# Kernel tuning notes

Hardware: AMD Instinct MI355X
Metric: run time of the kernel (lower is better)

The kernel has to match this reference:

```python
import jax, jax.numpy as jnp
import numpy as np

B, N, IN_DIM, HID = 16, 2048, 128, 128
EPS = 1e-5


def _layer(x, W, b, g, beta):
    # x: (B, N, d_in) -> (B, N, HID)
    h = jnp.einsum('bnd,dh->bnh', x, W) + b
    mu = jnp.mean(h, axis=-1, keepdims=True)
    var = jnp.mean((h - mu) ** 2, axis=-1, keepdims=True)
    h = (h - mu) * jax.lax.rsqrt(var + EPS) * g + beta
    return jax.nn.relu(h)


def setup_inputs() -> dict:
    key = jax.random.key(0)
    ks = jax.random.split(key, 8)
    x = jax.random.normal(ks[0], (B, N, IN_DIM), dtype=jnp.float32)
    adj = jax.random.uniform(ks[1], (B, N, N), dtype=jnp.float32)
    inp = {'x': x, 'adj': adj}
    dims = [IN_DIM, HID, HID]
    for i in range(3):
        d_in = dims[i]
        scale = 1.0 / np.sqrt(d_in)
        inp[f'W{i}'] = jax.random.uniform(ks[2 + i], (d_in, HID), dtype=jnp.float32, minval=-scale, maxval=scale)
        inp[f'b{i}'] = jax.random.uniform(ks[5 + i], (HID,), dtype=jnp.float32, minval=-scale, maxval=scale)
        inp[f'g{i}'] = jnp.ones((HID,), dtype=jnp.float32)
        inp[f'be{i}'] = jnp.zeros((HID,), dtype=jnp.float32)
    return inp


def reference(x, adj, W0, b0, g0, be0, W1, b1, g1, be1, W2, b2, g2, be2):
    params = [(W0, b0, g0, be0), (W1, b1, g1, be1), (W2, b2, g2, be2)]
    h = x
    for (W, b, g, beta) in params:
        h_agg = jnp.einsum('bnm,bmd->bnd', adj, h)  # dense adjacency aggregation
        h = _layer(h_agg, W, b, g, beta)
    return h
```

## Files before the change

kernel.cpp:

```cpp
#include <hip/hip_runtime.h>
#include <hip/hip_bf16.h>

typedef __bf16 bf16;
typedef __bf16 bf16x4 __attribute__((ext_vector_type(4)));
typedef __bf16 bf16x8 __attribute__((ext_vector_type(8)));
typedef float  f32x4  __attribute__((ext_vector_type(4)));

static constexpr int NB   = 16;
static constexpr int NN   = 2048;
static constexpr int HID  = 128;

__global__ __launch_bounds__(256) void prep_wt(const float* __restrict__ W0,
                                               const float* __restrict__ W1,
                                               const float* __restrict__ W2,
                                               bf16* __restrict__ WT) {
    int l = blockIdx.x;
    const float* W = (l == 0) ? W0 : (l == 1) ? W1 : W2;
    bf16* out = WT + l * 128 * 128;
    int tid = threadIdx.x;
#pragma unroll
    for (int i = 0; i < 64; ++i) {
        int idx = i * 256 + tid;
        int k = idx >> 7, n = idx & 127;
        out[n * 128 + k] = (bf16)W[idx];
    }
}

template<typename TA>
__global__ __launch_bounds__(256) void small_gemm(const TA* __restrict__ A,
                                                  const bf16* __restrict__ WT,
                                                  bf16* __restrict__ tmpT) {
    __shared__ bf16 smem[2 * 128 * 72];
    bf16* As = smem;
    bf16* Bs = smem + 128 * 72;

    const int tid  = threadIdx.x;
    const int wave = tid >> 6, lane = tid & 63;
    const int c0 = lane & 15, q = lane >> 4;
    const int blk = blockIdx.x;
    const int row_g0 = blk * 128;

    f32x4 acc[2][8] = {};

    for (int kk = 0; kk < 2; ++kk) {
        const int k0 = kk * 64;
        if constexpr (sizeof(TA) == 4) {
#pragma unroll
            for (int i = 0; i < 8; ++i) {
                int flat = i * 1024 + tid * 4;
                int row = flat >> 6, col = flat & 63;
                f32x4 v = *(const f32x4*)(A + (size_t)(row_g0 + row) * 128 + k0 + col);
                bf16x4 o = { (bf16)v.x, (bf16)v.y, (bf16)v.z, (bf16)v.w };
                *(bf16x4*)(As + row * 72 + col) = o;
            }
        } else {
#pragma unroll
            for (int i = 0; i < 4; ++i) {
                int flat = i * 2048 + tid * 8;
                int row = flat >> 6, col = flat & 63;
                bf16x8 v = *(const bf16x8*)((const bf16*)A + (size_t)(row_g0 + row) * 128 + k0 + col);
                *(bf16x8*)(As + row * 72 + col) = v;
            }
        }
#pragma unroll
        for (int i = 0; i < 4; ++i) {
            int flat = i * 2048 + tid * 8;
            int row = flat >> 6, col = flat & 63;
            bf16x8 v = *(const bf16x8*)(WT + (size_t)row * 128 + k0 + col);
            *(bf16x8*)(Bs + row * 72 + col) = v;
        }
        __syncthreads();
#pragma unroll
        for (int ks = 0; ks < 2; ++ks) {
            bf16x8 af[2];
#pragma unroll
            for (int mt = 0; mt < 2; ++mt)
                af[mt] = *(const bf16x8*)(As + (wave * 32 + mt * 16 + c0) * 72 + ks * 32 + q * 8);
#pragma unroll
            for (int nt = 0; nt < 8; ++nt) {
                bf16x8 bfr = *(const bf16x8*)(Bs + (nt * 16 + c0) * 72 + ks * 32 + q * 8);
#pragma unroll
                for (int mt = 0; mt < 2; ++mt)
                    acc[mt][nt] = __builtin_amdgcn_mfma_f32_16x16x32_bf16(af[mt], bfr, acc[mt][nt], 0, 0, 0);
            }
        }
        __syncthreads();
    }

    bf16* Cs = smem;
#pragma unroll
    for (int mt = 0; mt < 2; ++mt) {
        int mbase = wave * 32 + mt * 16 + q * 4;
#pragma unroll
        for (int nt = 0; nt < 8; ++nt) {
            int n = nt * 16 + c0;
#pragma unroll
            for (int r = 0; r < 4; ++r)
                Cs[n * 136 + mbase + r] = (bf16)acc[mt][nt][r];
        }
    }
    __syncthreads();
    const int b    = blk >> 4;
    const int row0 = (blk & 15) * 128;
    bf16* outp = tmpT + (size_t)b * 128 * 2048;
#pragma unroll
    for (int i = 0; i < 8; ++i) {
        int flat = i * 2048 + tid * 8;
        int n = flat >> 7, m = flat & 127;
        bf16x8 v = *(const bf16x8*)(Cs + n * 136 + m);
        *(bf16x8*)(outp + (size_t)n * 2048 + row0 + m) = v;
    }
}

template<int AMODE, bool OUTF32>
__global__ __launch_bounds__(256) void big_gemm(const float* __restrict__ Af,
                                                bf16* __restrict__ adjB,
                                                const bf16* __restrict__ Bt,
                                                const float* __restrict__ bias,
                                                const float* __restrict__ gamma,
                                                const float* __restrict__ betap,
                                                bf16* __restrict__ outB,
                                                float* __restrict__ outF) {
    __shared__ bf16 As[128 * 72];
    __shared__ bf16 Bs[128 * 72];

    const int tid  = threadIdx.x;
    const int wave = tid >> 6, lane = tid & 63;
    const int c0 = lane & 15, q = lane >> 4;
    const int b  = blockIdx.z;
    const int m0 = blockIdx.x * 128;
    const size_t abase = (size_t)b * 2048 * 2048;
    const bf16* Btb = Bt + (size_t)b * 128 * 2048;

    f32x4 acc[2][8] = {};

    for (int kk = 0; kk < 32; ++kk) {
        const int k0 = kk * 64;
        if constexpr (AMODE <= 1) {
#pragma unroll
            for (int i = 0; i < 8; ++i) {
                int flat = i * 1024 + tid * 4;
                int row = flat >> 6, col = flat & 63;
                f32x4 v = *(const f32x4*)(Af + abase + (size_t)(m0 + row) * 2048 + k0 + col);
                bf16x4 o = { (bf16)v.x, (bf16)v.y, (bf16)v.z, (bf16)v.w };
                *(bf16x4*)(As + row * 72 + col) = o;
                if constexpr (AMODE == 1)
                    *(bf16x4*)(adjB + abase + (size_t)(m0 + row) * 2048 + k0 + col) = o;
            }
        } else {
#pragma unroll
            for (int i = 0; i < 4; ++i) {
                int flat = i * 2048 + tid * 8;
                int row = flat >> 6, col = flat & 63;
                bf16x8 v = *(const bf16x8*)(adjB + abase + (size_t)(m0 + row) * 2048 + k0 + col);
                *(bf16x8*)(As + row * 72 + col) = v;
            }
        }
#pragma unroll
        for (int i = 0; i < 4; ++i) {
            int flat = i * 2048 + tid * 8;
            int row = flat >> 6, col = flat & 63;
            bf16x8 v = *(const bf16x8*)(Btb + (size_t)row * 2048 + k0 + col);
            *(bf16x8*)(Bs + row * 72 + col) = v;
        }
        __syncthreads();
#pragma unroll
        for (int ks = 0; ks < 2; ++ks) {
            bf16x8 af[2];
#pragma unroll
            for (int mt = 0; mt < 2; ++mt)
                af[mt] = *(const bf16x8*)(As + (wave * 32 + mt * 16 + c0) * 72 + ks * 32 + q * 8);
#pragma unroll
            for (int nt = 0; nt < 8; ++nt) {
                bf16x8 bfr = *(const bf16x8*)(Bs + (nt * 16 + c0) * 72 + ks * 32 + q * 8);
#pragma unroll
                for (int mt = 0; mt < 2; ++mt)
                    acc[mt][nt] = __builtin_amdgcn_mfma_f32_16x16x32_bf16(af[mt], bfr, acc[mt][nt], 0, 0, 0);
            }
        }
        __syncthreads();
    }

    float bv[8], gv[8], bev[8];
#pragma unroll
    for (int nt = 0; nt < 8; ++nt) {
        int n = nt * 16 + c0;
        bv[nt] = bias[n]; gv[nt] = gamma[n]; bev[nt] = betap[n];
    }
#pragma unroll
    for (int mt = 0; mt < 2; ++mt) {
#pragma unroll
        for (int r = 0; r < 4; ++r) {
            float s1 = 0.f, s2 = 0.f;
            float v[8];
#pragma unroll
            for (int nt = 0; nt < 8; ++nt) {
                float x = acc[mt][nt][r] + bv[nt];
                v[nt] = x; s1 += x; s2 += x * x;
            }
#pragma unroll
            for (int off = 1; off < 16; off <<= 1) {
                s1 += __shfl_xor(s1, off);
                s2 += __shfl_xor(s2, off);
            }
            float mu  = s1 * (1.f / 128.f);
            float var = s2 * (1.f / 128.f) - mu * mu;
            float rs  = rsqrtf(var + 1e-5f);
            int m = m0 + wave * 32 + mt * 16 + q * 4 + r;
            size_t rowoff = ((size_t)b * 2048 + m) * 128;
#pragma unroll
            for (int nt = 0; nt < 8; ++nt) {
                int n = nt * 16 + c0;
                float o = (v[nt] - mu) * rs * gv[nt] + bev[nt];
                o = fmaxf(o, 0.f);
                if constexpr (OUTF32) outF[rowoff + n] = o;
                else                  outB[rowoff + n] = (bf16)o;
            }
        }
    }
}

extern "C" void kernel_launch(void* const* d_in, const int* in_sizes, int n_in,
                              void* d_out, int out_size, void* d_ws, size_t ws_size,
                              hipStream_t stream) {
    const float* x   = (const float*)d_in[0];
    const float* adj = (const float*)d_in[1];
    const float* W[3]  = {(const float*)d_in[2],  (const float*)d_in[6],  (const float*)d_in[10]};
    const float* bb[3] = {(const float*)d_in[3],  (const float*)d_in[7],  (const float*)d_in[11]};
    const float* gg[3] = {(const float*)d_in[4],  (const float*)d_in[8],  (const float*)d_in[12]};
    const float* be[3] = {(const float*)d_in[5],  (const float*)d_in[9],  (const float*)d_in[13]};

    char* ws = (char*)d_ws;
    size_t off = 0;
    bf16* WT   = (bf16*)(ws + off); off += (size_t)3 * 128 * 128 * 2;
    off = (off + 255) & ~(size_t)255;
    bf16* tmpT = (bf16*)(ws + off); off += (size_t)NB * 128 * NN * 2;
    bf16* hB   = (bf16*)(ws + off); off += (size_t)NB * NN * 128 * 2;
    bf16* adjB = (bf16*)(ws + off); off += (size_t)NB * NN * NN * 2;
    const bool use_adjB = (ws_size >= off);

    float* outF = (float*)d_out;

    prep_wt<<<3, 256, 0, stream>>>(W[0], W[1], W[2], WT);

    dim3 bg(16, 1, 16);
    small_gemm<float><<<256, 256, 0, stream>>>(x, WT, tmpT);
    if (use_adjB)
        big_gemm<1, false><<<bg, 256, 0, stream>>>(adj, adjB, tmpT, bb[0], gg[0], be[0], hB, nullptr);
    else
        big_gemm<0, false><<<bg, 256, 0, stream>>>(adj, adjB, tmpT, bb[0], gg[0], be[0], hB, nullptr);
    small_gemm<bf16><<<256, 256, 0, stream>>>(hB, WT + 128 * 128, tmpT);
    if (use_adjB)
        big_gemm<2, false><<<bg, 256, 0, stream>>>(adj, adjB, tmpT, bb[1], gg[1], be[1], hB, nullptr);
    else
        big_gemm<0, false><<<bg, 256, 0, stream>>>(adj, adjB, tmpT, bb[1], gg[1], be[1], hB, nullptr);
    small_gemm<bf16><<<256, 256, 0, stream>>>(hB, WT + 2 * 128 * 128, tmpT);
    if (use_adjB)
        big_gemm<2, true><<<bg, 256, 0, stream>>>(adj, adjB, tmpT, bb[2], gg[2], be[2], nullptr, outF);
    else
        big_gemm<0, true><<<bg, 256, 0, stream>>>(adj, adjB, tmpT, bb[2], gg[2], be[2], nullptr, outF);
}
```

Measured before the change: 585.4 us.

## Split-K big GEMM with direct-to-LDS loads, swizzled LDS, separate reduce+LayerNorm

The adjacency is now converted to bf16 once in a dedicated pass. The big aggregation GEMM splits K in two across blockIdx.y, which doubles the grid from 256 to 512 blocks on a 256-CU part. It loads tiles with global_load_lds into an XOR-swizzled LDS layout and uses a 2x2 wave tiling with 4x4 MFMA fragments per wave. Partial sums go to an fp32 workspace, and a new reduce kernel adds the two halves and applies bias, LayerNorm and ReLU. This adds fp32 partial-sum traffic, extra launches and a larger workspace requirement, and it drops the fallback for the case where the workspace is too small.

```diff
diff --git a/kernel.cpp b/kernel.cpp
--- a/kernel.cpp
+++ b/kernel.cpp
@@ -4,11 +4,31 @@
 typedef __bf16 bf16;
 typedef __bf16 bf16x4 __attribute__((ext_vector_type(4)));
 typedef __bf16 bf16x8 __attribute__((ext_vector_type(8)));
+typedef float  f32x2  __attribute__((ext_vector_type(2)));
 typedef float  f32x4  __attribute__((ext_vector_type(4)));
 
-static constexpr int NB   = 16;
-static constexpr int NN   = 2048;
-static constexpr int HID  = 128;
+static constexpr int NB  = 16;
+static constexpr int NN  = 2048;
+static constexpr int HID = 128;
+
+__device__ __forceinline__ void gload_lds16(const bf16* g, bf16* l) {
+    __builtin_amdgcn_global_load_lds(
+        (const __attribute__((address_space(1))) unsigned int*)g,
+        (__attribute__((address_space(3))) unsigned int*)l, 16, 0, 0);
+}
+
+__global__ __launch_bounds__(256) void convert_adj(const float* __restrict__ A,
+                                                   bf16* __restrict__ B, long n8) {
+    long i = (long)blockIdx.x * blockDim.x + threadIdx.x;
+    long stride = (long)gridDim.x * blockDim.x;
+    for (; i < n8; i += stride) {
+        f32x4 a = *(const f32x4*)(A + i * 8);
+        f32x4 b = *(const f32x4*)(A + i * 8 + 4);
+        bf16x8 o = {(bf16)a.x, (bf16)a.y, (bf16)a.z, (bf16)a.w,
+                    (bf16)b.x, (bf16)b.y, (bf16)b.z, (bf16)b.w};
+        *(bf16x8*)(B + i * 8) = o;
+    }
+}
 
 __global__ __launch_bounds__(256) void prep_wt(const float* __restrict__ W0,
                                                const float* __restrict__ W1,
@@ -112,111 +132,112 @@
     }
 }
 
-template<int AMODE, bool OUTF32>
-__global__ __launch_bounds__(256) void big_gemm(const float* __restrict__ Af,
-                                                bf16* __restrict__ adjB,
-                                                const bf16* __restrict__ Bt,
-                                                const float* __restrict__ bias,
-                                                const float* __restrict__ gamma,
-                                                const float* __restrict__ betap,
-                                                bf16* __restrict__ outB,
-                                                float* __restrict__ outF) {
-    __shared__ bf16 As[128 * 72];
-    __shared__ bf16 Bs[128 * 72];
+__global__ __launch_bounds__(256, 2) void big_gemm(const bf16* __restrict__ adjB,
+                                                   const bf16* __restrict__ Bt,
+                                                   float* __restrict__ part) {
+    __shared__ bf16 As[128 * 64];
+    __shared__ bf16 Bs[128 * 64];
 
     const int tid  = threadIdx.x;
     const int wave = tid >> 6, lane = tid & 63;
     const int c0 = lane & 15, q = lane >> 4;
-    const int b  = blockIdx.z;
-    const int m0 = blockIdx.x * 128;
-    const size_t abase = (size_t)b * 2048 * 2048;
-    const bf16* Btb = Bt + (size_t)b * 128 * 2048;
-
-    f32x4 acc[2][8] = {};
-
-    for (int kk = 0; kk < 32; ++kk) {
-        const int k0 = kk * 64;
-        if constexpr (AMODE <= 1) {
-#pragma unroll
-            for (int i = 0; i < 8; ++i) {
-                int flat = i * 1024 + tid * 4;
-                int row = flat >> 6, col = flat & 63;
-                f32x4 v = *(const f32x4*)(Af + abase + (size_t)(m0 + row) * 2048 + k0 + col);
-                bf16x4 o = { (bf16)v.x, (bf16)v.y, (bf16)v.z, (bf16)v.w };
-                *(bf16x4*)(As + row * 72 + col) = o;
-                if constexpr (AMODE == 1)
-                    *(bf16x4*)(adjB + abase + (size_t)(m0 + row) * 2048 + k0 + col) = o;
-            }
-        } else {
-#pragma unroll
-            for (int i = 0; i < 4; ++i) {
-                int flat = i * 2048 + tid * 8;
-                int row = flat >> 6, col = flat & 63;
-                bf16x8 v = *(const bf16x8*)(adjB + abase + (size_t)(m0 + row) * 2048 + k0 + col);
-                *(bf16x8*)(As + row * 72 + col) = v;
-            }
-        }
-#pragma unroll
-        for (int i = 0; i < 4; ++i) {
-            int flat = i * 2048 + tid * 8;
-            int row = flat >> 6, col = flat & 63;
-            bf16x8 v = *(const bf16x8*)(Btb + (size_t)row * 2048 + k0 + col);
-            *(bf16x8*)(Bs + row * 72 + col) = v;
+    const int m0  = blockIdx.x * 128;
+    const int ksp = blockIdx.y;
+    const int b   = blockIdx.z;
+    const size_t abase = (size_t)b * NN * NN;
+    const bf16* Btb = Bt + (size_t)b * HID * NN;
+    const int mrow = (wave >> 1) * 64, ncol = (wave & 1) * 64;
+
+    f32x4 acc[4][4] = {};
+
+    int prow[4], pcb[4];
+#pragma unroll
+    for (int j = 0; j < 4; ++j) {
+        int p = j * 256 + wave * 64 + lane;
+        prow[j] = p >> 3;
+        pcb[j]  = (p & 7) ^ (prow[j] & 7);
+    }
+    const int ldsbase = wave * 64 * 8;
+
+    for (int kk = 0; kk < 16; ++kk) {
+        const int k0 = ksp * 1024 + kk * 64;
+#pragma unroll
+        for (int j = 0; j < 4; ++j) {
+            gload_lds16(adjB + abase + (size_t)(m0 + prow[j]) * NN + k0 + pcb[j] * 8,
+                        As + j * 2048 + ldsbase);
+            gload_lds16(Btb + (size_t)prow[j] * NN + k0 + pcb[j] * 8,
+                        Bs + j * 2048 + ldsbase);
         }
         __syncthreads();
 #pragma unroll
         for (int ks = 0; ks < 2; ++ks) {
-            bf16x8 af[2];
-#pragma unroll
-            for (int mt = 0; mt < 2; ++mt)
-                af[mt] = *(const bf16x8*)(As + (wave * 32 + mt * 16 + c0) * 72 + ks * 32 + q * 8);
-#pragma unroll
-            for (int nt = 0; nt < 8; ++nt) {
-                bf16x8 bfr = *(const bf16x8*)(Bs + (nt * 16 + c0) * 72 + ks * 32 + q * 8);
-#pragma unroll
-                for (int mt = 0; mt < 2; ++mt)
-                    acc[mt][nt] = __builtin_amdgcn_mfma_f32_16x16x32_bf16(af[mt], bfr, acc[mt][nt], 0, 0, 0);
-            }
-        }
-        __syncthreads();
-    }
-
-    float bv[8], gv[8], bev[8];
-#pragma unroll
-    for (int nt = 0; nt < 8; ++nt) {
-        int n = nt * 16 + c0;
-        bv[nt] = bias[n]; gv[nt] = gamma[n]; bev[nt] = betap[n];
-    }
-#pragma unroll
-    for (int mt = 0; mt < 2; ++mt) {
+            bf16x8 af[4], bfr[4];
+#pragma unroll
+            for (int mt = 0; mt < 4; ++mt) {
+                int row = mrow + mt * 16 + c0;
+                int cb  = (ks * 4 + q) ^ (row & 7);
+                af[mt] = *(const bf16x8*)(As + row * 64 + cb * 8);
+            }
+#pragma unroll
+            for (int nt = 0; nt < 4; ++nt) {
+                int row = ncol + nt * 16 + c0;
+                int cb  = (ks * 4 + q) ^ (row & 7);
+                bfr[nt] = *(const bf16x8*)(Bs + row * 64 + cb * 8);
+            }
+#pragma unroll
+            for (int mt = 0; mt < 4; ++mt)
+#pragma unroll
+                for (int nt = 0; nt < 4; ++nt)
+                    acc[mt][nt] = __builtin_amdgcn_mfma_f32_16x16x32_bf16(af[mt], bfr[nt], acc[mt][nt], 0, 0, 0);
+        }
+        __syncthreads();
+    }
+
+    float* pb = part + ((size_t)(ksp * NB + b) * NN + m0) * HID;
+#pragma unroll
+    for (int mt = 0; mt < 4; ++mt)
 #pragma unroll
         for (int r = 0; r < 4; ++r) {
-            float s1 = 0.f, s2 = 0.f;
-            float v[8];
-#pragma unroll
-            for (int nt = 0; nt < 8; ++nt) {
-                float x = acc[mt][nt][r] + bv[nt];
-                v[nt] = x; s1 += x; s2 += x * x;
-            }
-#pragma unroll
-            for (int off = 1; off < 16; off <<= 1) {
-                s1 += __shfl_xor(s1, off);
-                s2 += __shfl_xor(s2, off);
-            }
-            float mu  = s1 * (1.f / 128.f);
-            float var = s2 * (1.f / 128.f) - mu * mu;
-            float rs  = rsqrtf(var + 1e-5f);
-            int m = m0 + wave * 32 + mt * 16 + q * 4 + r;
-            size_t rowoff = ((size_t)b * 2048 + m) * 128;
-#pragma unroll
-            for (int nt = 0; nt < 8; ++nt) {
-                int n = nt * 16 + c0;
-                float o = (v[nt] - mu) * rs * gv[nt] + bev[nt];
-                o = fmaxf(o, 0.f);
-                if constexpr (OUTF32) outF[rowoff + n] = o;
-                else                  outB[rowoff + n] = (bf16)o;
-            }
-        }
+            int m = mrow + mt * 16 + q * 4 + r;
+#pragma unroll
+            for (int nt = 0; nt < 4; ++nt) {
+                int n = ncol + nt * 16 + c0;
+                pb[(size_t)m * HID + n] = acc[mt][nt][r];
+            }
+        }
+}
+
+template<bool OUTF32>
+__global__ __launch_bounds__(256) void reduce_ln(const float* __restrict__ part,
+                                                 const float* __restrict__ bias,
+                                                 const float* __restrict__ gamma,
+                                                 const float* __restrict__ betap,
+                                                 bf16* __restrict__ outB,
+                                                 float* __restrict__ outF) {
+    const int tid = threadIdx.x, wave = tid >> 6, lane = tid & 63;
+    const size_t row = (size_t)blockIdx.x * 4 + wave;
+    const size_t off = row * HID + lane * 2;
+    f32x2 p0 = *(const f32x2*)(part + off);
+    f32x2 p1 = *(const f32x2*)(part + (size_t)NB * NN * HID + off);
+    f32x2 bv = *(const f32x2*)(bias + lane * 2);
+    float x0 = p0.x + p1.x + bv.x;
+    float x1 = p0.y + p1.y + bv.y;
+    float s1 = x0 + x1, s2 = x0 * x0 + x1 * x1;
+#pragma unroll
+    for (int o = 1; o < 64; o <<= 1) { s1 += __shfl_xor(s1, o); s2 += __shfl_xor(s2, o); }
+    float mu  = s1 * (1.f / 128.f);
+    float var = s2 * (1.f / 128.f) - mu * mu;
+    float rs  = rsqrtf(var + 1e-5f);
+    f32x2 gv = *(const f32x2*)(gamma + lane * 2);
+    f32x2 be = *(const f32x2*)(betap + lane * 2);
+    float o0 = fmaxf((x0 - mu) * rs * gv.x + be.x, 0.f);
+    float o1 = fmaxf((x1 - mu) * rs * gv.y + be.y, 0.f);
+    if constexpr (OUTF32) {
+        f32x2 o = {o0, o1};
+        *(f32x2*)(outF + off) = o;
+    } else {
+        bf16* p = outB + off;
+        p[0] = (bf16)o0; p[1] = (bf16)o1;
     }
 }
 
@@ -232,31 +253,26 @@
 
     char* ws = (char*)d_ws;
     size_t off = 0;
-    bf16* WT   = (bf16*)(ws + off); off += (size_t)3 * 128 * 128 * 2;
-    off = (off + 255) & ~(size_t)255;
-    bf16* tmpT = (bf16*)(ws + off); off += (size_t)NB * 128 * NN * 2;
-    bf16* hB   = (bf16*)(ws + off); off += (size_t)NB * NN * 128 * 2;
-    bf16* adjB = (bf16*)(ws + off); off += (size_t)NB * NN * NN * 2;
-    const bool use_adjB = (ws_size >= off);
+    auto alloc = [&](size_t bytes) { char* p = ws + off; off = (off + bytes + 255) & ~(size_t)255; return p; };
+    bf16*  WT   = (bf16*) alloc((size_t)3 * 128 * 128 * 2);
+    bf16*  tmpT = (bf16*) alloc((size_t)NB * HID * NN * 2);
+    bf16*  hB   = (bf16*) alloc((size_t)NB * NN * HID * 2);
+    bf16*  adjB = (bf16*) alloc((size_t)NB * NN * NN * 2);
+    float* part = (float*)alloc((size_t)2 * NB * NN * HID * 4);
 
     float* outF = (float*)d_out;
 
     prep_wt<<<3, 256, 0, stream>>>(W[0], W[1], W[2], WT);
-
-    dim3 bg(16, 1, 16);
+    convert_adj<<<8192, 256, 0, stream>>>(adj, adjB, (long)NB * NN * NN / 8);
+
+    dim3 bg(16, 2, 16);
     small_gemm<float><<<256, 256, 0, stream>>>(x, WT, tmpT);
-    if (use_adjB)
-        big_gemm<1, false><<<bg, 256, 0, stream>>>(adj, adjB, tmpT, bb[0], gg[0], be[0], hB, nullptr);
-    else
-        big_gemm<0, false><<<bg, 256, 0, stream>>>(adj, adjB, tmpT, bb[0], gg[0], be[0], hB, nullptr);
+    big_gemm<<<bg, 256, 0, stream>>>(adjB, tmpT, part);
+    reduce_ln<false><<<8192, 256, 0, stream>>>(part, bb[0], gg[0], be[0], hB, nullptr);
     small_gemm<bf16><<<256, 256, 0, stream>>>(hB, WT + 128 * 128, tmpT);
-    if (use_adjB)
-        big_gemm<2, false><<<bg, 256, 0, stream>>>(adj, adjB, tmpT, bb[1], gg[1], be[1], hB, nullptr);
-    else
-        big_gemm<0, false><<<bg, 256, 0, stream>>>(adj, adjB, tmpT, bb[1], gg[1], be[1], hB, nullptr);
+    big_gemm<<<bg, 256, 0, stream>>>(adjB, tmpT, part);
+    reduce_ln<false><<<8192, 256, 0, stream>>>(part, bb[1], gg[1], be[1], hB, nullptr);
     small_gemm<bf16><<<256, 256, 0, stream>>>(hB, WT + 2 * 128 * 128, tmpT);
-    if (use_adjB)
-        big_gemm<2, true><<<bg, 256, 0, stream>>>(adj, adjB, tmpT, bb[2], gg[2], be[2], nullptr, outF);
-    else
-        big_gemm<0, true><<<bg, 256, 0, stream>>>(adj, adjB, tmpT, bb[2], gg[2], be[2], nullptr, outF);
-}
+    big_gemm<<<bg, 256, 0, stream>>>(adjB, tmpT, part);
+    reduce_ln<true><<<8192, 256, 0, stream>>>(part, bb[2], gg[2], be[2], nullptr, outF);
+}
```

Result: no change. 589.8 us (+0.8%).
